# Performance work log

Hardware: AMD Instinct MI355X
Metric: run time of the kernel (lower is better)

## Reference

```python
import jax, jax.numpy as jnp
import numpy as np
from jax import lax

NUM_CLASSES = 80
TOPK = 13
ALPHA = 1.0
BETA = 6.0
EPS = 1e-9
P = 150000
N = 256


def _make_boxes(key, n, scale):
    k1, k2 = jax.random.split(key)
    xy = jax.random.uniform(k1, (n, 2), dtype=jnp.float32) * scale
    wh = jax.random.uniform(k2, (n, 2), dtype=jnp.float32) * (0.2 * scale) + 1.0
    return jnp.concatenate([xy, xy + wh], axis=-1)  # valid x1y1x2y2


def setup_inputs() -> dict:
    key = jax.random.key(0)
    k1, k2, k3, k4 = jax.random.split(key, 4)
    cls_pred = jax.random.uniform(k1, (P, NUM_CLASSES), dtype=jnp.float32)
    bbox_pred = _make_boxes(k2, P, 640.0)
    bbox_gt = _make_boxes(k3, N, 640.0)
    # FG labels are > 0 (code indexes cls_pred[label-1])
    label_gt = jax.random.randint(k4, (N, 1), 1, NUM_CLASSES + 1, dtype=jnp.int32)
    return {"cls_pred": cls_pred, "bbox_pred": bbox_pred, "label_gt": label_gt, "bbox_gt": bbox_gt}


def _ious(bbox1, bbox2, eps=EPS):
    # bbox1: (N,4) gt, bbox2: (P,4) pred -> (N,P)
    b1 = bbox1[:, None, :]
    b2 = bbox2[None, :, :]
    x1y1 = jnp.maximum(b1[..., 0:2], b2[..., 0:2])
    x2y2 = jnp.minimum(b1[..., 2:4], b2[..., 2:4])
    inter = jnp.clip(x2y2 - x1y1, 0.0).prod(-1)
    area1 = jnp.clip(b1[..., 2:4] - b1[..., 0:2], 0.0).prod(-1)
    area2 = jnp.clip(b2[..., 2:4] - b2[..., 0:2], 0.0).prod(-1)
    return inter / (area1 + area2 - inter + eps)


def _metrics_topk(metrics, topk, eps=EPS):
    n, num_priors = metrics.shape
    topk_vals, topk_idxs = lax.top_k(metrics, topk)  # (N,k)
    keep = topk_vals.max(axis=-1, keepdims=True) > eps
    topk_idxs = jnp.where(keep, topk_idxs, 0)
    rows = jnp.arange(n)[:, None]
    counts = jnp.zeros((n, num_priors), jnp.int32).at[rows, topk_idxs].add(1)
    is_in_topk = jnp.where(counts > 1, 0, counts)
    return is_in_topk.astype(metrics.dtype)


def reference(cls_pred, bbox_pred, label_gt, bbox_gt):
    num_priors, num_classes = cls_pred.shape
    n_gt = bbox_gt.shape[0]
    ious = _ious(bbox_gt, bbox_pred)  # (N,P)
    lbl = label_gt.reshape(-1).astype(jnp.int32)  # (N,)
    bbox_cls_scores = jnp.take(cls_pred.T, lbl - 1, axis=0)  # (N,P)
    alignment_metrics = jnp.power(bbox_cls_scores, ALPHA) * jnp.power(ious, BETA)
    mask_positive = _metrics_topk(alignment_metrics, TOPK)  # (N,P) float 0/1
    mask_positive_sum = mask_positive.sum(axis=0)  # (P,)
    # conflict resolution: priors claimed by >1 gt go to the max-iou gt.
    # Applying unconditionally equals the torch data-dependent branch.
    is_max_iou = (jnp.arange(n_gt)[:, None] == ious.argmax(axis=0)[None, :]).astype(ious.dtype)
    mask_positive = jnp.where(mask_positive_sum[None, :] > 1, is_max_iou, mask_positive)
    mask_positive_sum = mask_positive.sum(axis=0)
    assigned_gt_index = mask_positive.argmax(axis=0)  # (P,)
    assigned_labels = lbl[assigned_gt_index]  # (P,)
    assigned_cls = jax.nn.one_hot(assigned_labels - 1, num_classes, dtype=jnp.int32)
    assigned_bboxes = bbox_gt[assigned_gt_index]  # (P,4)
    assigned_labels = jnp.where(mask_positive_sum > 0, assigned_labels, 0)
    return (assigned_gt_index, assigned_labels, assigned_cls, assigned_bboxes)
```

## Files before the change

kernel.cpp:

```cpp
#include <hip/hip_runtime.h>

#define TOPK 13
#define NCLS 80
#define EPSF 1e-9f
#define NSEG 32
#define GPB  8
#define CAP3 512
#define MCAP (64 * TOPK)

__global__ __launch_bounds__(256) void setup(const int* __restrict__ lbl,
                                             int* __restrict__ count,
                                             int* __restrict__ firstg,
                                             int* __restrict__ gorder, int P, int N) {
    int t = threadIdx.x;
    if (blockIdx.x == 0) {
        __shared__ int key[256];
        key[t] = (t < N) ? ((lbl[t] << 8) | t) : 0x7FFFFFFF;
        __syncthreads();
        for (int k = 2; k <= 256; k <<= 1) {
            for (int j = k >> 1; j >= 1; j >>= 1) {
                int ixj = t ^ j;
                if (ixj > t) {
                    int a = key[t], b = key[ixj];
                    bool up = ((t & k) == 0);
                    if (up ? (a > b) : (a < b)) { key[t] = b; key[ixj] = a; }
                }
                __syncthreads();
            }
        }
        if (t < N) gorder[t] = key[t] & 0xFF;
    } else {
        int base = (blockIdx.x - 1) * 1024 + t * 4;
        if (base + 3 < P) {
            *(int4*)&count[base]  = make_int4(0, 0, 0, 0);
            *(int4*)&firstg[base] = make_int4(0x7FFFFFFF, 0x7FFFFFFF, 0x7FFFFFFF, 0x7FFFFFFF);
        } else {
            for (int i = base; i < P; i++) { count[i] = 0; firstg[i] = 0x7FFFFFFF; }
        }
    }
}

__global__ __launch_bounds__(512, 4) void phaseA1(const float* __restrict__ cls,
                                                  const float4* __restrict__ bboxp,
                                                  const float4* __restrict__ bboxg,
                                                  const int* __restrict__ lbl,
                                                  const int* __restrict__ gorder,
                                                  float2* __restrict__ cand,
                                                  int P, int N, int seglen) {
#pragma clang fp contract(off)
    const int s = blockIdx.x, tile = blockIdx.y, t = threadIdx.x;
    const int wv = t >> 6, lane = t & 63;
    const int pstart = s * seglen;
    int pend = pstart + seglen; if (pend > P) pend = P;

    __shared__ int pbuf[GPB][CAP3];
    __shared__ float2 mbuf[GPB][MCAP];
    __shared__ int ctr[GPB];

    float4 gb[GPB];
#pragma unroll
    for (int j = 0; j < GPB; j++) {
        int gi8 = tile * GPB + j;
        int gj = (gi8 < N) ? gorder[gi8] : -1;
        gb[j] = (gj >= 0) ? bboxg[gj] : make_float4(0.f, 0.f, 0.f, 0.f);
    }
    if (t < GPB) ctr[t] = 0;
    __syncthreads();

    bool first = true;
    for (int p = pstart + t; p < pend; p += 512) {
        float4 pb = bboxp[p];
        bool force = first && (t < 16);
        first = false;
#pragma unroll
        for (int j = 0; j < GPB; j++) {
            float dx = fminf(gb[j].z, pb.z) - fmaxf(gb[j].x, pb.x);
            float dy = fminf(gb[j].w, pb.w) - fmaxf(gb[j].y, pb.y);
            bool want = ((dx > 0.0f) && (dy > 0.0f)) || force;
            if (want) {
                int slot = atomicAdd(&ctr[j], 1);
                if (slot < CAP3) pbuf[j][slot] = p;
            }
        }
    }
    __syncthreads();

    const int gi8 = tile * GPB + wv;
    const bool myValid = gi8 < N;
    const int gj = myValid ? gorder[gi8] : 0;
    const float4 gbw = bboxg[gj];
    const float gaw = fmaxf(gbw.z - gbw.x, 0.0f) * fmaxf(gbw.w - gbw.y, 0.0f);
    const int cidx = lbl[gj] - 1;
    const int rawtotal = ctr[wv];

    float v[TOPK]; int id[TOPK];
#pragma unroll
    for (int k = 0; k < TOPK; k++) { v[k] = -1.0f; id[k] = 0x7FFFFFFF; }

    auto ins = [&](float m, int p) {
        bool b12 = (m > v[TOPK - 1]) || (m == v[TOPK - 1] && p < id[TOPK - 1]);
        if (b12) {
#pragma unroll
            for (int k = TOPK - 1; k >= 1; k--) {
                bool a = (m > v[k - 1]) || (m == v[k - 1] && p < id[k - 1]);
                bool b = (m > v[k]) || (m == v[k] && p < id[k]);
                float nv = a ? v[k - 1] : (b ? m : v[k]);
                int   ni = a ? id[k - 1] : (b ? p : id[k]);
                v[k] = nv; id[k] = ni;
            }
            bool a0 = (m > v[0]) || (m == v[0] && p < id[0]);
            if (a0) { v[0] = m; id[0] = p; }
        }
    };

    if (rawtotal <= CAP3) {
        for (int e = lane; e < rawtotal; e += 64) {
            int pp = pbuf[wv][e];
            float4 pb = bboxp[pp];
            float sc = cls[(size_t)pp * NCLS + cidx];
            float pa = fmaxf(pb.z - pb.x, 0.0f) * fmaxf(pb.w - pb.y, 0.0f);
            float xx1 = fmaxf(gbw.x, pb.x), yy1 = fmaxf(gbw.y, pb.y);
            float xx2 = fminf(gbw.z, pb.z), yy2 = fminf(gbw.w, pb.w);
            float inter = fmaxf(xx2 - xx1, 0.0f) * fmaxf(yy2 - yy1, 0.0f);
            float iou = inter / (((gaw + pa) - inter) + EPSF);
            float i2 = iou * iou;
            float m = sc * ((i2 * i2) * i2);
            ins(m, pp);
        }
    } else if (myValid) {
        for (int pp = pstart + lane; pp < pend; pp += 64) {
            float4 pb = bboxp[pp];
            float sc = cls[(size_t)pp * NCLS + cidx];
            float pa = fmaxf(pb.z - pb.x, 0.0f) * fmaxf(pb.w - pb.y, 0.0f);
            float xx1 = fmaxf(gbw.x, pb.x), yy1 = fmaxf(gbw.y, pb.y);
            float xx2 = fminf(gbw.z, pb.z), yy2 = fminf(gbw.w, pb.w);
            float inter = fmaxf(xx2 - xx1, 0.0f) * fmaxf(yy2 - yy1, 0.0f);
            float iou = inter / (((gaw + pa) - inter) + EPSF);
            float i2 = iou * iou;
            float m = sc * ((i2 * i2) * i2);
            ins(m, pp);
        }
    }

    float2* wl = mbuf[wv];
#pragma unroll
    for (int k = 0; k < TOPK; k++)
        wl[lane * TOPK + k] = make_float2(v[k], __int_as_float(id[k]));
    __syncthreads();
    for (int str = 32; str >= 1; str >>= 1) {
        if (lane < str) {
            float2 merged[TOPK];
            int a = 0, b = 0;
            const int ba = lane * TOPK, bb = (lane + str) * TOPK;
#pragma unroll
            for (int k = 0; k < TOPK; k++) {
                float2 fa = wl[ba + a], fb = wl[bb + b];
                int ia = __float_as_int(fa.y), ib = __float_as_int(fb.y);
                bool takeA = (fa.x > fb.x) || (fa.x == fb.x && ia < ib);
                merged[k] = takeA ? fa : fb;
                a += takeA; b += !takeA;
            }
#pragma unroll
            for (int k = 0; k < TOPK; k++) wl[ba + k] = merged[k];
        }
        __syncthreads();
    }
    if (lane < TOPK && myValid)
        cand[((size_t)gj * NSEG + s) * TOPK + lane] = wl[lane];
}

__global__ __launch_bounds__(512) void phaseA2(const float2* __restrict__ cand,
                                               int* __restrict__ count,
                                               int* __restrict__ firstg) {
    const int g = blockIdx.x;
    const int t = threadIdx.x;
    const int M = NSEG * TOPK;
    __shared__ float cv[512];
    __shared__ int   ci[512];
    if (t < M) {
        float2 e = cand[(size_t)g * M + t];
        cv[t] = e.x; ci[t] = __float_as_int(e.y);
    } else {
        cv[t] = -1.0f; ci[t] = 0x7FFFFFFF;
    }
    __syncthreads();
    for (int k = 2; k <= 512; k <<= 1) {
        for (int j = k >> 1; j >= 1; j >>= 1) {
            int ixj = t ^ j;
            if (ixj > t) {
                float va = cv[t], vb = cv[ixj];
                int   ia = ci[t], ib = ci[ixj];
                bool aBeforeB = (va > vb) || (va == vb && ia < ib);
                bool dirFwd = ((t & k) == 0);
                bool doswap = dirFwd ? !aBeforeB : aBeforeB;
                if (doswap) { cv[t] = vb; ci[t] = ib; cv[ixj] = va; ci[ixj] = ia; }
            }
            __syncthreads();
        }
    }
    if (t < TOPK && cv[0] > EPSF) {
        int pi = ci[t];
        atomicAdd(&count[pi], 1);
        atomicMin(&firstg[pi], g);
    }
}

__global__ __launch_bounds__(256) void phaseCF(const float4* __restrict__ bboxp,
                                               const float4* __restrict__ bboxg,
                                               const int* __restrict__ lbl,
                                               const int* __restrict__ count,
                                               const int* __restrict__ firstg,
                                               float* __restrict__ out0,
                                               float* __restrict__ out1,
                                               float4* __restrict__ outcls4,
                                               float4* __restrict__ outbox4, int P, int N) {
#pragma clang fp contract(off)
    __shared__ float4 gbS[256];
    __shared__ int glS[256];
    __shared__ int clsl[256];
    int t = threadIdx.x;
    if (t < N) { gbS[t] = bboxg[t]; glS[t] = lbl[t]; }
    __syncthreads();
    int p0 = blockIdx.x * 256;
    int nloc = P - p0; if (nloc > 256) nloc = 256;
    if (t < nloc) {
        int p = p0 + t;
        int cnt = count[p];
        int gi = 0, pos = 0;
        if (cnt == 1) { gi = firstg[p]; pos = 1; }
        else if (cnt > 1) {
            float4 pb = bboxp[p];
            float pa = fmaxf(pb.z - pb.x, 0.0f) * fmaxf(pb.w - pb.y, 0.0f);
            float best = -1.0f;
            for (int g = 0; g < N; g++) {
                float4 g4 = gbS[g];
                float gar = fmaxf(g4.z - g4.x, 0.0f) * fmaxf(g4.w - g4.y, 0.0f);
                float xx1 = fmaxf(g4.x, pb.x), yy1 = fmaxf(g4.y, pb.y);
                float xx2 = fminf(g4.z, pb.z), yy2 = fminf(g4.w, pb.w);
                float inter = fmaxf(xx2 - xx1, 0.0f) * fmaxf(yy2 - yy1, 0.0f);
                float iou = inter / (((gar + pa) - inter) + EPSF);
                if (iou > best) { best = iou; gi = g; }
            }
            pos = 1;
        }
        out0[p] = (float)gi;
        out1[p] = pos ? (float)glS[gi] : 0.0f;
        clsl[t] = glS[gi] - 1;
        outbox4[p] = gbS[gi];
    }
    __syncthreads();
    for (int f = t; f < nloc * 20; f += 256) {
        int pl = f / 20, q = f - pl * 20;
        int cl = clsl[pl], c0 = q * 4;
        float4 vv = make_float4(c0 == cl ? 1.0f : 0.0f, c0 + 1 == cl ? 1.0f : 0.0f,
                                c0 + 2 == cl ? 1.0f : 0.0f, c0 + 3 == cl ? 1.0f : 0.0f);
        outcls4[(size_t)p0 * 20 + f] = vv;
    }
}

__global__ __launch_bounds__(256) void phaseC1(const float4* __restrict__ bboxp,
                                               const float4* __restrict__ bboxg,
                                               const int* __restrict__ lbl,
                                               const int* __restrict__ count,
                                               const int* __restrict__ firstg,
                                               float* __restrict__ out0,
                                               float* __restrict__ out1, int P, int N) {
#pragma clang fp contract(off)
    __shared__ float4 gbS[256];
    __shared__ int glS[256];
    if (threadIdx.x < (unsigned)N) {
        gbS[threadIdx.x] = bboxg[threadIdx.x];
        glS[threadIdx.x] = lbl[threadIdx.x];
    }
    __syncthreads();
    int p = blockIdx.x * 256 + threadIdx.x;
    if (p >= P) return;
    int cnt = count[p];
    int gi = 0, pos = 0;
    if (cnt == 1) { gi = firstg[p]; pos = 1; }
    else if (cnt > 1) {
        float4 pb = bboxp[p];
        float pa = fmaxf(pb.z - pb.x, 0.0f) * fmaxf(pb.w - pb.y, 0.0f);
        float best = -1.0f;
        for (int g = 0; g < N; g++) {
            float4 g4 = gbS[g];
            float gar = fmaxf(g4.z - g4.x, 0.0f) * fmaxf(g4.w - g4.y, 0.0f);
            float xx1 = fmaxf(g4.x, pb.x), yy1 = fmaxf(g4.y, pb.y);
            float xx2 = fminf(g4.z, pb.z), yy2 = fminf(g4.w, pb.w);
            float inter = fmaxf(xx2 - xx1, 0.0f) * fmaxf(yy2 - yy1, 0.0f);
            float iou = inter / (((gar + pa) - inter) + EPSF);
            if (iou > best) { best = iou; gi = g; }
        }
        pos = 1;
    }
    out0[p] = (float)gi;
    out1[p] = pos ? (float)glS[gi] : 0.0f;
}

__global__ __launch_bounds__(256) void phaseC2(const float4* __restrict__ bboxg,
                                               const int* __restrict__ lbl,
                                               const float* __restrict__ out0,
                                               float* __restrict__ outcls,
                                               float* __restrict__ outbox, int P, int N) {
    __shared__ float gbb[256 * 4];
    __shared__ int glS[256];
    __shared__ int clsl[256];
    __shared__ int gil[256];
    int tid = threadIdx.x;
    if (tid < N) {
        float4 b = bboxg[tid];
        gbb[tid * 4 + 0] = b.x; gbb[tid * 4 + 1] = b.y;
        gbb[tid * 4 + 2] = b.z; gbb[tid * 4 + 3] = b.w;
        glS[tid] = lbl[tid];
    }
    __syncthreads();
    int p0 = blockIdx.x * 256;
    int nloc = P - p0; if (nloc > 256) nloc = 256;
    if (tid < nloc) {
        int gi = (int)out0[p0 + tid];
        gil[tid] = gi;
        clsl[tid] = glS[gi] - 1;
    }
    __syncthreads();
    for (int f = tid; f < nloc * NCLS; f += 256) {
        int pl = f / NCLS;
        int c  = f - pl * NCLS;
        outcls[(size_t)p0 * NCLS + f] = (c == clsl[pl]) ? 1.0f : 0.0f;
    }
    for (int f = tid; f < nloc * 4; f += 256) {
        int pl = f >> 2, k = f & 3;
        outbox[(size_t)p0 * 4 + f] = gbb[gil[pl] * 4 + k];
    }
}

extern "C" void kernel_launch(void* const* d_in, const int* in_sizes, int n_in,
                              void* d_out, int out_size, void* d_ws, size_t ws_size,
                              hipStream_t stream) {
    const float* cls_pred  = (const float*)d_in[0];
    const float* bbox_pred = (const float*)d_in[1];
    const int*   label_gt  = (const int*)d_in[2];
    const float* bbox_gt   = (const float*)d_in[3];
    int P = in_sizes[1] / 4;
    int N = in_sizes[3] / 4;

    float* out    = (float*)d_out;
    float* out0   = out;
    float* out1   = out + (size_t)P;
    float* outcls = out + (size_t)2 * P;
    float* outbox = out + (size_t)82 * P;

    int pb = (P + 255) / 256;
    int seglen = (P + NSEG - 1) / NSEG;
    int gtiles = (N + GPB - 1) / GPB;
    dim3 gridA1(NSEG, gtiles);
    int setupBlocks = 1 + (P + 1023) / 1024;
    size_t candBytes = (size_t)N * NSEG * TOPK * sizeof(float2);
    size_t needWs = (size_t)P * 8 + candBytes + (size_t)N * 4 + 64;

    if (ws_size >= needWs) {
        int*    count  = (int*)d_ws;
        int*    firstg = count + P;
        float2* cand   = (float2*)(firstg + P);
        int*    gorder = (int*)((char*)cand + candBytes);

        setup<<<setupBlocks, 256, 0, stream>>>(label_gt, count, firstg, gorder, P, N);
        phaseA1<<<gridA1, 512, 0, stream>>>(cls_pred, (const float4*)bbox_pred,
                                            (const float4*)bbox_gt, label_gt, gorder,
                                            cand, P, N, seglen);
        phaseA2<<<N, 512, 0, stream>>>(cand, count, firstg);
        phaseCF<<<pb, 256, 0, stream>>>((const float4*)bbox_pred, (const float4*)bbox_gt,
                                        label_gt, count, firstg, out0, out1,
                                        (float4*)outcls, (float4*)outbox, P, N);
    } else {
        int*    count  = (int*)outbox;
        int*    firstg = ((int*)outbox) + P;
        float2* cand   = (float2*)(((int*)outbox) + 2 * (size_t)P);
        int*    gorder = (int*)((char*)cand + candBytes);

        setup<<<setupBlocks, 256, 0, stream>>>(label_gt, count, firstg, gorder, P, N);
        phaseA1<<<gridA1, 512, 0, stream>>>(cls_pred, (const float4*)bbox_pred,
                                            (const float4*)bbox_gt, label_gt, gorder,
                                            cand, P, N, seglen);
        phaseC1<<<pb, 256, 0, stream>>>((const float4*)bbox_pred, (const float4*)bbox_gt,
                                        label_gt, count, firstg, out0, out1, P, N);
        phaseC2<<<pb, 256, 0, stream>>>((const float4*)bbox_gt, label_gt, out0,
                                        outcls, outbox, P, N);
    }
}
```

Baseline: 219.7 us.

## Alias candidate buffer into merge buffer, unroll overlap scan, raise occupancy

The per-group candidate index buffer now shares shared memory with the top-k merge buffer, separated by an extra barrier. That cut in LDS footprint lets launch bounds request 6 blocks per CU instead of 4, and the segment count drops from 32 to 24. The overlap-test loop is unrolled to issue four prior-box loads before testing them, to hide memory latency. The costs are more register pressure under the tighter bound, longer per-block segments that may overflow the capacity fallback more often, and one added barrier.

```diff
diff --git a/kernel.cpp b/kernel.cpp
--- a/kernel.cpp
+++ b/kernel.cpp
@@ -3,7 +3,7 @@
 #define TOPK 13
 #define NCLS 80
 #define EPSF 1e-9f
-#define NSEG 32
+#define NSEG 24
 #define GPB  8
 #define CAP3 512
 #define MCAP (64 * TOPK)
@@ -40,7 +40,7 @@
     }
 }
 
-__global__ __launch_bounds__(512, 4) void phaseA1(const float* __restrict__ cls,
+__global__ __launch_bounds__(512, 6) void phaseA1(const float* __restrict__ cls,
                                                   const float4* __restrict__ bboxp,
                                                   const float4* __restrict__ bboxg,
                                                   const int* __restrict__ lbl,
@@ -53,9 +53,9 @@
     const int pstart = s * seglen;
     int pend = pstart + seglen; if (pend > P) pend = P;
 
-    __shared__ int pbuf[GPB][CAP3];
     __shared__ float2 mbuf[GPB][MCAP];
     __shared__ int ctr[GPB];
+    int* pbuf = (int*)&mbuf[0][0];
 
     float4 gb[GPB];
 #pragma unroll
@@ -67,11 +67,7 @@
     if (t < GPB) ctr[t] = 0;
     __syncthreads();
 
-    bool first = true;
-    for (int p = pstart + t; p < pend; p += 512) {
-        float4 pb = bboxp[p];
-        bool force = first && (t < 16);
-        first = false;
+    auto testapp = [&](float4 pb, int p, bool force) {
 #pragma unroll
         for (int j = 0; j < GPB; j++) {
             float dx = fminf(gb[j].z, pb.z) - fmaxf(gb[j].x, pb.x);
@@ -79,10 +75,24 @@
             bool want = ((dx > 0.0f) && (dy > 0.0f)) || force;
             if (want) {
                 int slot = atomicAdd(&ctr[j], 1);
-                if (slot < CAP3) pbuf[j][slot] = p;
-            }
-        }
-    }
+                if (slot < CAP3) pbuf[j * CAP3 + slot] = p;
+            }
+        }
+    };
+
+    int p = pstart + t;
+    if (p < pend) { testapp(bboxp[p], p, t < 16); p += 512; }
+    for (; p + 1536 < pend; p += 2048) {
+        float4 pb0 = bboxp[p];
+        float4 pb1 = bboxp[p + 512];
+        float4 pb2 = bboxp[p + 1024];
+        float4 pb3 = bboxp[p + 1536];
+        testapp(pb0, p, false);
+        testapp(pb1, p + 512, false);
+        testapp(pb2, p + 1024, false);
+        testapp(pb3, p + 1536, false);
+    }
+    for (; p < pend; p += 512) testapp(bboxp[p], p, false);
     __syncthreads();
 
     const int gi8 = tile * GPB + wv;
@@ -97,25 +107,25 @@
 #pragma unroll
     for (int k = 0; k < TOPK; k++) { v[k] = -1.0f; id[k] = 0x7FFFFFFF; }
 
-    auto ins = [&](float m, int p) {
-        bool b12 = (m > v[TOPK - 1]) || (m == v[TOPK - 1] && p < id[TOPK - 1]);
+    auto ins = [&](float m, int pp) {
+        bool b12 = (m > v[TOPK - 1]) || (m == v[TOPK - 1] && pp < id[TOPK - 1]);
         if (b12) {
 #pragma unroll
             for (int k = TOPK - 1; k >= 1; k--) {
-                bool a = (m > v[k - 1]) || (m == v[k - 1] && p < id[k - 1]);
-                bool b = (m > v[k]) || (m == v[k] && p < id[k]);
+                bool a = (m > v[k - 1]) || (m == v[k - 1] && pp < id[k - 1]);
+                bool b = (m > v[k]) || (m == v[k] && pp < id[k]);
                 float nv = a ? v[k - 1] : (b ? m : v[k]);
-                int   ni = a ? id[k - 1] : (b ? p : id[k]);
+                int   ni = a ? id[k - 1] : (b ? pp : id[k]);
                 v[k] = nv; id[k] = ni;
             }
-            bool a0 = (m > v[0]) || (m == v[0] && p < id[0]);
-            if (a0) { v[0] = m; id[0] = p; }
+            bool a0 = (m > v[0]) || (m == v[0] && pp < id[0]);
+            if (a0) { v[0] = m; id[0] = pp; }
         }
     };
 
     if (rawtotal <= CAP3) {
         for (int e = lane; e < rawtotal; e += 64) {
-            int pp = pbuf[wv][e];
+            int pp = pbuf[wv * CAP3 + e];
             float4 pb = bboxp[pp];
             float sc = cls[(size_t)pp * NCLS + cidx];
             float pa = fmaxf(pb.z - pb.x, 0.0f) * fmaxf(pb.w - pb.y, 0.0f);
@@ -141,6 +151,7 @@
             ins(m, pp);
         }
     }
+    __syncthreads();
 
     float2* wl = mbuf[wv];
 #pragma unroll
```

Result: slower. 315.6 us (+43.7%).

## Double segments per GT and replace bitonic sort with per-thread top-k plus merge tree

Applied to the files above, without the earlier changes.

Raises the number of prior segments per ground-truth box from 32 to 64, which gives phaseA1 more parallel blocks. phaseA2 has to combine 64*13 candidates, more than its 512 threads, so the full bitonic sort is replaced by a per-thread insertion top-k followed by a shared-memory pairwise merge tree. The fallback path now stores candidates in the class output buffer and adds the missing phaseA2 launch, which reads as a correctness fix. The costs are a larger candidate buffer and a sizeable shared-memory footprint in phaseA2, about 52 KB.

```diff
diff --git a/kernel.cpp b/kernel.cpp
--- a/kernel.cpp
+++ b/kernel.cpp
@@ -3,7 +3,7 @@
 #define TOPK 13
 #define NCLS 80
 #define EPSF 1e-9f
-#define NSEG 32
+#define NSEG 64
 #define GPB  8
 #define CAP3 512
 #define MCAP (64 * TOPK)
@@ -97,19 +97,19 @@
 #pragma unroll
     for (int k = 0; k < TOPK; k++) { v[k] = -1.0f; id[k] = 0x7FFFFFFF; }
 
-    auto ins = [&](float m, int p) {
-        bool b12 = (m > v[TOPK - 1]) || (m == v[TOPK - 1] && p < id[TOPK - 1]);
+    auto ins = [&](float m, int pp) {
+        bool b12 = (m > v[TOPK - 1]) || (m == v[TOPK - 1] && pp < id[TOPK - 1]);
         if (b12) {
 #pragma unroll
             for (int k = TOPK - 1; k >= 1; k--) {
-                bool a = (m > v[k - 1]) || (m == v[k - 1] && p < id[k - 1]);
-                bool b = (m > v[k]) || (m == v[k] && p < id[k]);
+                bool a = (m > v[k - 1]) || (m == v[k - 1] && pp < id[k - 1]);
+                bool b = (m > v[k]) || (m == v[k] && pp < id[k]);
                 float nv = a ? v[k - 1] : (b ? m : v[k]);
-                int   ni = a ? id[k - 1] : (b ? p : id[k]);
+                int   ni = a ? id[k - 1] : (b ? pp : id[k]);
                 v[k] = nv; id[k] = ni;
             }
-            bool a0 = (m > v[0]) || (m == v[0] && p < id[0]);
-            if (a0) { v[0] = m; id[0] = p; }
+            bool a0 = (m > v[0]) || (m == v[0] && pp < id[0]);
+            if (a0) { v[0] = m; id[0] = pp; }
         }
     };
 
@@ -175,31 +175,57 @@
     const int g = blockIdx.x;
     const int t = threadIdx.x;
     const int M = NSEG * TOPK;
-    __shared__ float cv[512];
-    __shared__ int   ci[512];
-    if (t < M) {
-        float2 e = cand[(size_t)g * M + t];
-        cv[t] = e.x; ci[t] = __float_as_int(e.y);
-    } else {
-        cv[t] = -1.0f; ci[t] = 0x7FFFFFFF;
-    }
-    __syncthreads();
-    for (int k = 2; k <= 512; k <<= 1) {
-        for (int j = k >> 1; j >= 1; j >>= 1) {
-            int ixj = t ^ j;
-            if (ixj > t) {
-                float va = cv[t], vb = cv[ixj];
-                int   ia = ci[t], ib = ci[ixj];
-                bool aBeforeB = (va > vb) || (va == vb && ia < ib);
-                bool dirFwd = ((t & k) == 0);
-                bool doswap = dirFwd ? !aBeforeB : aBeforeB;
-                if (doswap) { cv[t] = vb; ci[t] = ib; cv[ixj] = va; ci[ixj] = ia; }
-            }
-            __syncthreads();
-        }
-    }
-    if (t < TOPK && cv[0] > EPSF) {
-        int pi = ci[t];
+    float v[TOPK]; int id[TOPK];
+#pragma unroll
+    for (int k = 0; k < TOPK; k++) { v[k] = -1.0f; id[k] = 0x7FFFFFFF; }
+    for (int e = t; e < M; e += 512) {
+        float2 E = cand[(size_t)g * M + e];
+        float m = E.x; int pp = __float_as_int(E.y);
+        bool b12 = (m > v[TOPK - 1]) || (m == v[TOPK - 1] && pp < id[TOPK - 1]);
+        if (b12) {
+#pragma unroll
+            for (int k = TOPK - 1; k >= 1; k--) {
+                bool a = (m > v[k - 1]) || (m == v[k - 1] && pp < id[k - 1]);
+                bool b = (m > v[k]) || (m == v[k] && pp < id[k]);
+                float nv = a ? v[k - 1] : (b ? m : v[k]);
+                int   ni = a ? id[k - 1] : (b ? pp : id[k]);
+                v[k] = nv; id[k] = ni;
+            }
+            bool a0 = (m > v[0]) || (m == v[0] && pp < id[0]);
+            if (a0) { v[0] = m; id[0] = pp; }
+        }
+    }
+    __shared__ float sv[512 * TOPK];
+    __shared__ int   si[512 * TOPK];
+#pragma unroll
+    for (int k = 0; k < TOPK; k++) {
+        sv[t * TOPK + k] = v[k];
+        si[t * TOPK + k] = id[k];
+    }
+    __syncthreads();
+    for (int str = 256; str >= 1; str >>= 1) {
+        if (t < str) {
+            float* va = &sv[t * TOPK];
+            int*   ia = &si[t * TOPK];
+            float* vb = &sv[(t + str) * TOPK];
+            int*   ib = &si[(t + str) * TOPK];
+            float mv[TOPK]; int mi[TOPK];
+            int a = 0, b = 0;
+#pragma unroll
+            for (int k = 0; k < TOPK; k++) {
+                float fa = va[a], fb = vb[b];
+                int   xa = ia[a], xb = ib[b];
+                bool takeA = (fa > fb) || (fa == fb && xa < xb);
+                if (takeA) { mv[k] = fa; mi[k] = xa; a++; }
+                else       { mv[k] = fb; mi[k] = xb; b++; }
+            }
+#pragma unroll
+            for (int k = 0; k < TOPK; k++) { va[k] = mv[k]; ia[k] = mi[k]; }
+        }
+        __syncthreads();
+    }
+    if (t < TOPK && sv[0] > EPSF) {
+        int pi = si[t];
         atomicAdd(&count[pi], 1);
         atomicMin(&firstg[pi], g);
     }
@@ -374,13 +400,14 @@
     } else {
         int*    count  = (int*)outbox;
         int*    firstg = ((int*)outbox) + P;
-        float2* cand   = (float2*)(((int*)outbox) + 2 * (size_t)P);
+        float2* cand   = (float2*)outcls;
         int*    gorder = (int*)((char*)cand + candBytes);
 
         setup<<<setupBlocks, 256, 0, stream>>>(label_gt, count, firstg, gorder, P, N);
         phaseA1<<<gridA1, 512, 0, stream>>>(cls_pred, (const float4*)bbox_pred,
                                             (const float4*)bbox_gt, label_gt, gorder,
                                             cand, P, N, seglen);
+        phaseA2<<<N, 512, 0, stream>>>(cand, count, firstg);
         phaseC1<<<pb, 256, 0, stream>>>((const float4*)bbox_pred, (const float4*)bbox_gt,
                                         label_gt, count, firstg, out0, out1, P, N);
         phaseC2<<<pb, 256, 0, stream>>>((const float4*)bbox_gt, label_gt, out0,
```

Measured after the change: 248.6 us. 13.2% more time.
